# Optimization experiments

Hardware: AMD Instinct MI355X
Metric: run time of the kernel (lower is better)

## Reference

```python
import jax, jax.numpy as jnp
import numpy as np

K = 3       # attractive nearest neighbors
J = 3       # repulsive offset (uses dist[:, :, J:])
ALPHA = 0.1
NU = 1e-3


def setup_inputs() -> dict:
    key = jax.random.key(0)
    k1, k2 = jax.random.split(key, 2)
    phi_p = jax.random.normal(k1, (4, 512, 64, 64), dtype=jnp.float32)
    memory_bank = jax.random.normal(k2, (16384, 512), dtype=jnp.float32)
    r = jnp.ones((1,), dtype=jnp.float32)
    return {"phi_p": phi_p, "memory_bank": memory_bank, "r": r}


def reference(phi_p, memory_bank, r):
    B, C, H, W = phi_p.shape
    # b c h w -> b (h w) c
    x = phi_p.reshape(B, C, H * W).transpose(0, 2, 1)
    x2 = jnp.sum(x * x, axis=-1, keepdims=True)            # [B, HW, 1]
    m2 = jnp.sum(memory_bank * memory_bank, axis=-1)       # [N]
    d2 = x2 + m2[None, None, :] - 2.0 * jnp.einsum('bnc,mc->bnm', x, memory_bank)
    d2 = jnp.maximum(d2, 0.0)                              # [B, HW, N]
    # smallest K+J squared distances, ascending (topk(largest=False))
    neg_top, _ = jax.lax.top_k(-d2, K + J)
    dist = -neg_top                                        # [B, HW, K+J]
    r2 = r ** 2
    scores_att = dist[:, :, :K] - r2
    loss_att = jnp.mean(jnp.maximum(scores_att, 0.0)) / NU
    scores_rep = r2 - dist[:, :, J:] - ALPHA
    loss_rep = jnp.mean(jnp.maximum(scores_rep, 0.0)) / NU
    return loss_att + loss_rep
```

## Files before the change

### kernel.cpp

```cpp
#include <hip/hip_runtime.h>
#include <cfloat>

#define B_   4
#define C_   512
#define HW_  4096
#define R_   16384
#define N_   16384
#define ALPHA_ 0.1f
#define SCALE_ ((float)(1000.0/49152.0))

#define NCHUNK 4

typedef unsigned int u32;
typedef unsigned short u16;
typedef unsigned char u8;
typedef __attribute__((ext_vector_type(2))) unsigned long long u64x2;
typedef __attribute__((ext_vector_type(4))) float f32x4;

typedef const __attribute__((address_space(1))) u32* gas_u32;
typedef __attribute__((address_space(3))) u32* las_u32;

__device__ __forceinline__ void async16(const void* g, void* l) {
    __builtin_amdgcn_global_load_lds((gas_u32)g, (las_u32)l, 16, 0, 0);
}

__device__ __forceinline__ u32 pk_fp8x4(float a, float b, float c, float d) {
    u32 v = __builtin_amdgcn_cvt_pk_fp8_f32(a, b, 0, false);
    v = __builtin_amdgcn_cvt_pk_fp8_f32(c, d, v, true);
    return v;
}

__device__ __forceinline__ void ins6(float (&t)[6], float v) {
    if (v < t[5]) {
        t[5] = v;
        #pragma unroll
        for (int q = 5; q >= 1; --q) {
            float lo = fminf(t[q-1], t[q]);
            float hi = fmaxf(t[q-1], t[q]);
            t[q-1] = lo; t[q] = hi;
        }
    }
}

__global__ void conv_mem_kernel(const float* __restrict__ mem,
                                u8* __restrict__ Mb, float* __restrict__ m2) {
    int w = threadIdx.x >> 6, l = threadIdx.x & 63;
    int row = blockIdx.x * 4 + w;
    const float4* p = (const float4*)(mem + (size_t)row * C_);
    float4 a = p[l], b = p[l + 64];
    float s = a.x*a.x + a.y*a.y + a.z*a.z + a.w*a.w
            + b.x*b.x + b.y*b.y + b.z*b.z + b.w*b.w;
    *(u32*)(Mb + (size_t)row * C_ + l*4)       = pk_fp8x4(a.x, a.y, a.z, a.w);
    *(u32*)(Mb + (size_t)row * C_ + 256 + l*4) = pk_fp8x4(b.x, b.y, b.z, b.w);
    #pragma unroll
    for (int off = 32; off > 0; off >>= 1) s += __shfl_down(s, off);
    if (l == 0) m2[row] = s;
}

__global__ void conv_phi_kernel(const float* __restrict__ phi, u8* __restrict__ Xb,
                                float* __restrict__ x2) {
    __shared__ float T[64][65];
    int t = threadIdx.x;
    int n0 = blockIdx.x * 64, c0 = blockIdx.y * 64, b = blockIdx.z;
    const float* src = phi + ((size_t)b * C_ + c0) * HW_ + n0;
    int l = t & 63, cg = t >> 6;
    float sq = 0.f;
    #pragma unroll
    for (int p = 0; p < 16; ++p) {
        int c = cg + p * 4;
        float v = src[(size_t)c * HW_ + l];
        T[c][l] = v;
        sq = fmaf(v, v, sq);
    }
    atomicAdd(&x2[(size_t)b * HW_ + n0 + l], sq);
    __syncthreads();
    int cq = t & 15, gl0 = t >> 4;
    #pragma unroll
    for (int p = 0; p < 4; ++p) {
        int gl = gl0 + p * 16;
        u32 v = pk_fp8x4(T[cq*4+0][gl], T[cq*4+1][gl],
                         T[cq*4+2][gl], T[cq*4+3][gl]);
        size_t g = (size_t)b * HW_ + n0 + gl;
        *(u32*)(Xb + g * C_ + c0 + cq*4) = v;
    }
}

__global__ __launch_bounds__(256, 2) void gemm_topk_kernel(
    const u8* __restrict__ Xb, const u8* __restrict__ Mb,
    const float* __restrict__ m2, float* __restrict__ P ) {
    __shared__ __align__(16) u8 smem[24832];
    u8* Xs = smem;
    u8* Ms = smem + 8192;

    const int t = threadIdx.x;
    const int w = t >> 6, l = t & 63;
    const int g0  = blockIdx.x * 128;
    const int n0c = blockIdx.y * (N_ / NCHUNK);
    const int rh  = w * 32;
    const int fm  = l & 15;
    const int rq  = l >> 4;
    const int pc  = (rq ^ ((fm >> 1) & 3)) * 16;
    const int srow4 = l >> 2;
    const int soff  = (((l & 3) ^ ((l >> 3) & 3)) * 16);

    float top[8][6];
    #pragma unroll
    for (int s8 = 0; s8 < 8; ++s8)
        #pragma unroll
        for (int q = 0; q < 6; ++q) top[s8][q] = FLT_MAX;

    const u8* Xsrc = Xb + (size_t)(g0 + rh) * C_;
    u8* XsW = Xs + rh * 64;
    u8* MsW = Ms + rh * 64;

    for (int nt = 0; nt < N_ / NCHUNK / 128; ++nt) {
        const int n0 = n0c + nt * 128;
        const u8* Msrc = Mb + (size_t)(n0 + rh) * C_;

        float m2w[8];
        #pragma unroll
        for (int n = 0; n < 8; ++n) m2w[n] = m2[n0 + n * 16 + fm];

        f32x4 acc[2][8];
        #pragma unroll
        for (int m = 0; m < 2; ++m)
            #pragma unroll
            for (int n = 0; n < 8; ++n) acc[m][n] = (f32x4)0.f;

        for (int s = 0; s < 8; ++s) {
            const int k0 = s * 64;
            #pragma unroll
            for (int i = 0; i < 2; ++i) {
                async16(Xsrc + (size_t)(i*16 + srow4) * C_ + k0 + soff, XsW + i*1024);
                async16(Msrc + (size_t)(i*16 + srow4) * C_ + k0 + soff, MsW + i*1024);
            }
            __syncthreads();
            u64x2 av[2], bv[8];
            #pragma unroll
            for (int m = 0; m < 2; ++m)
                av[m] = *(const u64x2*)(Xs + (rh + m*16 + fm) * 64 + pc);
            #pragma unroll
            for (int n = 0; n < 8; ++n)
                bv[n] = *(const u64x2*)(Ms + (n*16 + fm) * 64 + pc);
            #pragma unroll
            for (int m = 0; m < 2; ++m)
                #pragma unroll
                for (int n = 0; n < 8; ++n)
                    acc[m][n] = __builtin_amdgcn_mfma_f32_16x16x32_fp8_fp8(
                        (long)av[m].x, (long)bv[n].x, acc[m][n], 0, 0, 0);
            #pragma unroll
            for (int m = 0; m < 2; ++m)
                #pragma unroll
                for (int n = 0; n < 8; ++n)
                    acc[m][n] = __builtin_amdgcn_mfma_f32_16x16x32_fp8_fp8(
                        (long)av[m].y, (long)bv[n].y, acc[m][n], 0, 0, 0);
            __syncthreads();
        }

        #pragma unroll
        for (int m = 0; m < 2; ++m)
            #pragma unroll
            for (int j = 0; j < 4; ++j) {
                float d0 = m2w[0] - 2.f * acc[m][0][j];
                float d1 = m2w[1] - 2.f * acc[m][1][j];
                float d2 = m2w[2] - 2.f * acc[m][2][j];
                float d3 = m2w[3] - 2.f * acc[m][3][j];
                float d4 = m2w[4] - 2.f * acc[m][4][j];
                float d5 = m2w[5] - 2.f * acc[m][5][j];
                float d6 = m2w[6] - 2.f * acc[m][6][j];
                float d7 = m2w[7] - 2.f * acc[m][7][j];
                float vmin = fminf(fminf(fminf(d0, d1), fminf(d2, d3)),
                                   fminf(fminf(d4, d5), fminf(d6, d7)));
                float (&tt)[6] = top[m * 4 + j];
                if (vmin < tt[5]) {
                    ins6(tt, d0); ins6(tt, d1); ins6(tt, d2); ins6(tt, d3);
                    ins6(tt, d4); ins6(tt, d5); ins6(tt, d6); ins6(tt, d7);
                }
            }
    }

    float* Mg = (float*)smem;
    #pragma unroll 1
    for (int p = 0; p < 2; ++p) {
        __syncthreads();
        if ((w >> 1) == p) {
            #pragma unroll
            for (int m = 0; m < 2; ++m)
                #pragma unroll
                for (int j = 0; j < 4; ++j) {
                    int lrow = (w & 1) * 32 + m * 16 + rq * 4 + j;
                    #pragma unroll
                    for (int q = 0; q < 6; ++q)
                        Mg[lrow * 97 + fm * 6 + q] = top[m * 4 + j][q];
                }
        }
        __syncthreads();
        if (t < 64) {
            float t6[6];
            #pragma unroll
            for (int q = 0; q < 6; ++q) t6[q] = FLT_MAX;
            const float* row = Mg + t * 97;
            for (int v = 0; v < 96; ++v) ins6(t6, row[v]);
            float* dst = P + ((size_t)(g0 + p * 64 + t) * NCHUNK + blockIdx.y) * 6;
            #pragma unroll
            for (int q = 0; q < 6; ++q) dst[q] = t6[q];
        }
    }
}

__global__ void finalize_kernel(const float* __restrict__ P, const float* __restrict__ x2,
                                const float* __restrict__ rp, float* __restrict__ out) {
    int g = blockIdx.x * 256 + threadIdx.x;
    float t6[6];
    #pragma unroll
    for (int q = 0; q < 6; ++q) t6[q] = FLT_MAX;
    const f32x4* pp = (const f32x4*)(P + (size_t)g * (NCHUNK * 6));
    #pragma unroll
    for (int q = 0; q < NCHUNK * 6 / 4; ++q) {
        f32x4 v = pp[q];
        ins6(t6, v.x); ins6(t6, v.y); ins6(t6, v.z); ins6(t6, v.w);
    }
    float x2g = x2[g];
    float rv = rp[0], r2 = rv * rv;
    float s = 0.f;
    #pragma unroll
    for (int i = 0; i < 3; ++i) {
        float d = fmaxf(t6[i] + x2g, 0.f);
        s += fmaxf(d - r2, 0.f);
    }
    #pragma unroll
    for (int i = 3; i < 6; ++i) {
        float d = fmaxf(t6[i] + x2g, 0.f);
        s += fmaxf(r2 - d - ALPHA_, 0.f);
    }
    #pragma unroll
    for (int off = 32; off > 0; off >>= 1) s += __shfl_down(s, off);
    __shared__ float red[4];
    int w = threadIdx.x >> 6, l = threadIdx.x & 63;
    if (l == 0) red[w] = s;
    __syncthreads();
    if (threadIdx.x == 0)
        atomicAdd(out, (red[0] + red[1] + red[2] + red[3]) * SCALE_);
}

#define TM 64
#define TN 64
#define KC 64
#define LDP 68

__global__ void m2_kernel(const float* __restrict__ mem, float* __restrict__ m2) {
    int wave = threadIdx.x >> 6, lane = threadIdx.x & 63;
    int row = blockIdx.x * 4 + wave;
    const float4* p = reinterpret_cast<const float4*>(mem + (size_t)row * C_);
    float4 a = p[lane], b = p[lane + 64];
    float s = a.x*a.x + a.y*a.y + a.z*a.z + a.w*a.w
            + b.x*b.x + b.y*b.y + b.z*b.z + b.w*b.w;
    #pragma unroll
    for (int off = 32; off > 0; off >>= 1) s += __shfl_down(s, off);
    if (lane == 0) m2[row] = s;
}

__global__ void x2f_kernel(const float* __restrict__ phi, float* __restrict__ x2) {
    int g = blockIdx.x * blockDim.x + threadIdx.x;
    int b = g >> 12;
    int n = g & 4095;
    const float* p = phi + (size_t)b * C_ * HW_ + n;
    float s = 0.f;
    #pragma unroll 8
    for (int c = 0; c < C_; ++c) {
        float v = p[(size_t)c * HW_];
        s = fmaf(v, v, s);
    }
    x2[g] = s;
}

__global__ __launch_bounds__(256) void dist_loss_kernel(
    const float* __restrict__ phi, const float* __restrict__ mem,
    const float* __restrict__ rp,  const float* __restrict__ m2,
    const float* __restrict__ x2,  float* __restrict__ out) {
    __shared__ float smem[2 * TM * LDP];
    float* xs = smem;
    float* ms = smem + TM * LDP;
    const int tid = threadIdx.x;
    const int tx = tid & 15, ty = tid >> 4;
    const int g0 = blockIdx.x * TM;
    const int b = g0 >> 12, n0img = g0 & 4095;
    const float* phiB = phi + (size_t)b * C_ * HW_ + n0img;
    float top[4][6];
    #pragma unroll
    for (int i = 0; i < 4; ++i)
        #pragma unroll
        for (int q = 0; q < 6; ++q) top[i][q] = FLT_MAX;
    float x2v[4];
    #pragma unroll
    for (int i = 0; i < 4; ++i) x2v[i] = x2[g0 + ty * 4 + i];
    for (int nt = 0; nt < N_ / TN; ++nt) {
        const int n0 = nt * TN;
        float acc[4][4];
        #pragma unroll
        for (int i = 0; i < 4; ++i)
            #pragma unroll
            for (int j = 0; j < 4; ++j) acc[i][j] = 0.f;
        for (int s = 0; s < C_ / KC; ++s) {
            const int k0 = s * KC;
            {
                int rr = tid & 63, cb = tid >> 6;
                #pragma unroll
                for (int p = 0; p < 16; ++p) {
                    int cc = p * 4 + cb;
                    xs[rr * LDP + cc] = phiB[(size_t)(k0 + cc) * HW_ + rr];
                }
            }
            {
                int kq = tid & 15, cb = tid >> 4;
                #pragma unroll
                for (int p = 0; p < 4; ++p) {
                    int c = p * 16 + cb;
                    float4 v = *reinterpret_cast<const float4*>(
                        mem + (size_t)(n0 + c) * C_ + k0 + kq * 4);
                    ms[(kq*4+0)*LDP + c] = v.x; ms[(kq*4+1)*LDP + c] = v.y;
                    ms[(kq*4+2)*LDP + c] = v.z; ms[(kq*4+3)*LDP + c] = v.w;
                }
            }
            __syncthreads();
            #pragma unroll
            for (int kq = 0; kq < KC / 4; ++kq) {
                float4 xa[4], mb[4];
                #pragma unroll
                for (int i = 0; i < 4; ++i)
                    xa[i] = *reinterpret_cast<const float4*>(&xs[(ty*4+i)*LDP + kq*4]);
                #pragma unroll
                for (int kk = 0; kk < 4; ++kk)
                    mb[kk] = *reinterpret_cast<const float4*>(&ms[(kq*4+kk)*LDP + tx*4]);
                #pragma unroll
                for (int i = 0; i < 4; ++i) {
                    const float xk[4] = {xa[i].x, xa[i].y, xa[i].z, xa[i].w};
                    #pragma unroll
                    for (int kk = 0; kk < 4; ++kk) {
                        const float mc[4] = {mb[kk].x, mb[kk].y, mb[kk].z, mb[kk].w};
                        #pragma unroll
                        for (int j = 0; j < 4; ++j)
                            acc[i][j] = fmaf(xk[kk], mc[j], acc[i][j]);
                    }
                }
            }
            __syncthreads();
        }
        #pragma unroll
        for (int j = 0; j < 4; ++j) {
            float m2v = m2[n0 + tx * 4 + j];
            #pragma unroll
            for (int i = 0; i < 4; ++i) {
                float d = fmaxf(x2v[i] + m2v - 2.f * acc[i][j], 0.f);
                ins6(top[i], d);
            }
        }
    }
    __syncthreads();
    float* mg = smem;
    #pragma unroll
    for (int i = 0; i < 4; ++i)
        #pragma unroll
        for (int q = 0; q < 6; ++q)
            mg[(ty*4+i)*97 + tx*6 + q] = top[i][q];
    __syncthreads();
    if (tid < 64) {
        float t6[6];
        #pragma unroll
        for (int q = 0; q < 6; ++q) t6[q] = FLT_MAX;
        const float* row = mg + tid * 97;
        for (int v = 0; v < 96; ++v) ins6(t6, row[v]);
        float rv = rp[0], r2 = rv * rv;
        float s = fmaxf(t6[0]-r2,0.f) + fmaxf(t6[1]-r2,0.f) + fmaxf(t6[2]-r2,0.f)
                + fmaxf(r2-t6[3]-ALPHA_,0.f) + fmaxf(r2-t6[4]-ALPHA_,0.f)
                + fmaxf(r2-t6[5]-ALPHA_,0.f);
        #pragma unroll
        for (int off = 32; off > 0; off >>= 1) s += __shfl_down(s, off);
        if (tid == 0) atomicAdd(out, s * SCALE_);
    }
}

extern "C" void kernel_launch(void* const* d_in, const int* in_sizes, int n_in,
                              void* d_out, int out_size, void* d_ws, size_t ws_size,
                              hipStream_t stream) {
    const float* phi = (const float*)d_in[0];
    const float* mem = (const float*)d_in[1];
    const float* rp  = (const float*)d_in[2];
    float* out = (float*)d_out;

    const size_t offX  = 0;
    const size_t offM  = (size_t)R_ * C_;
    const size_t offx2 = offM + (size_t)N_ * C_;
    const size_t offm2 = offx2 + (size_t)R_ * 4;
    const size_t offP  = offm2 + (size_t)N_ * 4;
    const size_t need  = offP + (size_t)R_ * NCHUNK * 6 * 4;

    hipMemsetAsync(out, 0, sizeof(float), stream);

    if (ws_size >= need) {
        u8*    Xb = (u8*)((char*)d_ws + offX);
        u8*    Mb = (u8*)((char*)d_ws + offM);
        float* x2 = (float*)((char*)d_ws + offx2);
        float* m2 = (float*)((char*)d_ws + offm2);
        float* P  = (float*)((char*)d_ws + offP);

        hipMemsetAsync(x2, 0, (size_t)R_ * 4, stream);
        conv_mem_kernel<<<N_ / 4, 256, 0, stream>>>(mem, Mb, m2);
        conv_phi_kernel<<<dim3(HW_ / 64, C_ / 64, B_), 256, 0, stream>>>(phi, Xb, x2);
        gemm_topk_kernel<<<dim3(128, NCHUNK), 256, 0, stream>>>(Xb, Mb, m2, P);
        finalize_kernel<<<R_ / 256, 256, 0, stream>>>(P, x2, rp, out);
    } else {
        float* m2 = (float*)d_ws;
        float* x2 = m2 + N_;
        m2_kernel<<<N_ / 4, 256, 0, stream>>>(mem, m2);
        x2f_kernel<<<R_ / 256, 256, 0, stream>>>(phi, x2);
        dist_loss_kernel<<<R_ / TM, 256, 0, stream>>>(phi, mem, rp, m2, x2, out);
    }
}
```

Before: 405.3 us.

## Swap MFMA operands so each lane owns a query row, shrink top-k state

Swaps the A/B operands of the fp8 MFMA so the accumulator layout gives each lane 4 consecutive memory-bank columns for a single query row. Each lane then keeps two top-6 lists instead of eight, which cuts register pressure. This allows launch bounds of 4 blocks per CU and a smaller shared buffer. NCHUNK doubles to 8 to expose more blocks, at the cost of a larger partial buffer and more work in the finalize pass. The m2 values are now read from global memory inside the epilogue rather than preloaded into registers.

New measurement: 451.7 us. 11.4% more time.

```diff
diff --git a/kernel.cpp b/kernel.cpp
--- a/kernel.cpp
+++ b/kernel.cpp
@@ -9,7 +9,7 @@
 #define ALPHA_ 0.1f
 #define SCALE_ ((float)(1000.0/49152.0))
 
-#define NCHUNK 4
+#define NCHUNK 8
 
 typedef unsigned int u32;
 typedef unsigned short u16;
@@ -85,10 +85,10 @@
     }
 }
 
-__global__ __launch_bounds__(256, 2) void gemm_topk_kernel(
+__global__ __launch_bounds__(256, 4) void gemm_topk_kernel(
     const u8* __restrict__ Xb, const u8* __restrict__ Mb,
     const float* __restrict__ m2, float* __restrict__ P ) {
-    __shared__ __align__(16) u8 smem[24832];
+    __shared__ __align__(16) u8 smem[16384];
     u8* Xs = smem;
     u8* Ms = smem + 8192;
 
@@ -103,11 +103,11 @@
     const int srow4 = l >> 2;
     const int soff  = (((l & 3) ^ ((l >> 3) & 3)) * 16);
 
-    float top[8][6];
-    #pragma unroll
-    for (int s8 = 0; s8 < 8; ++s8)
-        #pragma unroll
-        for (int q = 0; q < 6; ++q) top[s8][q] = FLT_MAX;
+    float top[2][6];
+    #pragma unroll
+    for (int m = 0; m < 2; ++m)
+        #pragma unroll
+        for (int q = 0; q < 6; ++q) top[m][q] = FLT_MAX;
 
     const u8* Xsrc = Xb + (size_t)(g0 + rh) * C_;
     u8* XsW = Xs + rh * 64;
@@ -117,15 +117,11 @@
         const int n0 = n0c + nt * 128;
         const u8* Msrc = Mb + (size_t)(n0 + rh) * C_;
 
-        float m2w[8];
-        #pragma unroll
-        for (int n = 0; n < 8; ++n) m2w[n] = m2[n0 + n * 16 + fm];
-
         f32x4 acc[2][8];
         #pragma unroll
         for (int m = 0; m < 2; ++m)
             #pragma unroll
-            for (int n = 0; n < 8; ++n) acc[m][n] = (f32x4)0.f;
+            for (int a = 0; a < 8; ++a) acc[m][a] = (f32x4)0.f;
 
         for (int s = 0; s < 8; ++s) {
             const int k0 = s * 64;
@@ -135,48 +131,52 @@
                 async16(Msrc + (size_t)(i*16 + srow4) * C_ + k0 + soff, MsW + i*1024);
             }
             __syncthreads();
-            u64x2 av[2], bv[8];
+            u64x2 xv[2];
             #pragma unroll
             for (int m = 0; m < 2; ++m)
-                av[m] = *(const u64x2*)(Xs + (rh + m*16 + fm) * 64 + pc);
-            #pragma unroll
-            for (int n = 0; n < 8; ++n)
-                bv[n] = *(const u64x2*)(Ms + (n*16 + fm) * 64 + pc);
-            #pragma unroll
-            for (int m = 0; m < 2; ++m)
-                #pragma unroll
-                for (int n = 0; n < 8; ++n)
-                    acc[m][n] = __builtin_amdgcn_mfma_f32_16x16x32_fp8_fp8(
-                        (long)av[m].x, (long)bv[n].x, acc[m][n], 0, 0, 0);
-            #pragma unroll
-            for (int m = 0; m < 2; ++m)
-                #pragma unroll
-                for (int n = 0; n < 8; ++n)
-                    acc[m][n] = __builtin_amdgcn_mfma_f32_16x16x32_fp8_fp8(
-                        (long)av[m].y, (long)bv[n].y, acc[m][n], 0, 0, 0);
+                xv[m] = *(const u64x2*)(Xs + (rh + m*16 + fm) * 64 + pc);
+            #pragma unroll
+            for (int a = 0; a < 8; ++a) {
+                u64x2 av = *(const u64x2*)(Ms + (a*16 + fm) * 64 + pc);
+                #pragma unroll
+                for (int m = 0; m < 2; ++m) {
+                    acc[m][a] = __builtin_amdgcn_mfma_f32_16x16x32_fp8_fp8(
+                        (long)av.x, (long)xv[m].x, acc[m][a], 0, 0, 0);
+                    acc[m][a] = __builtin_amdgcn_mfma_f32_16x16x32_fp8_fp8(
+                        (long)av.y, (long)xv[m].y, acc[m][a], 0, 0, 0);
+                }
+            }
             __syncthreads();
         }
 
-        #pragma unroll
-        for (int m = 0; m < 2; ++m)
-            #pragma unroll
-            for (int j = 0; j < 4; ++j) {
-                float d0 = m2w[0] - 2.f * acc[m][0][j];
-                float d1 = m2w[1] - 2.f * acc[m][1][j];
-                float d2 = m2w[2] - 2.f * acc[m][2][j];
-                float d3 = m2w[3] - 2.f * acc[m][3][j];
-                float d4 = m2w[4] - 2.f * acc[m][4][j];
-                float d5 = m2w[5] - 2.f * acc[m][5][j];
-                float d6 = m2w[6] - 2.f * acc[m][6][j];
-                float d7 = m2w[7] - 2.f * acc[m][7][j];
-                float vmin = fminf(fminf(fminf(d0, d1), fminf(d2, d3)),
-                                   fminf(fminf(d4, d5), fminf(d6, d7)));
-                float (&tt)[6] = top[m * 4 + j];
-                if (vmin < tt[5]) {
-                    ins6(tt, d0); ins6(tt, d1); ins6(tt, d2); ins6(tt, d3);
-                    ins6(tt, d4); ins6(tt, d5); ins6(tt, d6); ins6(tt, d7);
-                }
-            }
+        float vm0 = FLT_MAX, vm1 = FLT_MAX;
+        #pragma unroll
+        for (int a = 0; a < 8; ++a) {
+            float4 q = *(const float4*)(m2 + n0 + a * 16 + rq * 4);
+            f32x4 a0 = acc[0][a], a1 = acc[1][a];
+            vm0 = fminf(vm0, fminf(fminf(q.x - 2.f*a0.x, q.y - 2.f*a0.y),
+                                   fminf(q.z - 2.f*a0.z, q.w - 2.f*a0.w)));
+            vm1 = fminf(vm1, fminf(fminf(q.x - 2.f*a1.x, q.y - 2.f*a1.y),
+                                   fminf(q.z - 2.f*a1.z, q.w - 2.f*a1.w)));
+        }
+        if (vm0 < top[0][5]) {
+            #pragma unroll
+            for (int a = 0; a < 8; ++a) {
+                float4 q = *(const float4*)(m2 + n0 + a * 16 + rq * 4);
+                f32x4 a0 = acc[0][a];
+                ins6(top[0], q.x - 2.f*a0.x); ins6(top[0], q.y - 2.f*a0.y);
+                ins6(top[0], q.z - 2.f*a0.z); ins6(top[0], q.w - 2.f*a0.w);
+            }
+        }
+        if (vm1 < top[1][5]) {
+            #pragma unroll
+            for (int a = 0; a < 8; ++a) {
+                float4 q = *(const float4*)(m2 + n0 + a * 16 + rq * 4);
+                f32x4 a1 = acc[1][a];
+                ins6(top[1], q.x - 2.f*a1.x); ins6(top[1], q.y - 2.f*a1.y);
+                ins6(top[1], q.z - 2.f*a1.z); ins6(top[1], q.w - 2.f*a1.w);
+            }
+        }
     }
 
     float* Mg = (float*)smem;
@@ -185,22 +185,21 @@
         __syncthreads();
         if ((w >> 1) == p) {
             #pragma unroll
-            for (int m = 0; m < 2; ++m)
-                #pragma unroll
-                for (int j = 0; j < 4; ++j) {
-                    int lrow = (w & 1) * 32 + m * 16 + rq * 4 + j;
-                    #pragma unroll
-                    for (int q = 0; q < 6; ++q)
-                        Mg[lrow * 97 + fm * 6 + q] = top[m * 4 + j][q];
-                }
+            for (int m = 0; m < 2; ++m) {
+                int lrow = (w & 1) * 32 + m * 16 + fm;
+                #pragma unroll
+                for (int q = 0; q < 6; ++q)
+                    Mg[lrow * 25 + rq * 6 + q] = top[m][q];
+            }
         }
         __syncthreads();
         if (t < 64) {
             float t6[6];
             #pragma unroll
             for (int q = 0; q < 6; ++q) t6[q] = FLT_MAX;
-            const float* row = Mg + t * 97;
-            for (int v = 0; v < 96; ++v) ins6(t6, row[v]);
+            const float* row = Mg + t * 25;
+            #pragma unroll
+            for (int v = 0; v < 24; ++v) ins6(t6, row[v]);
             float* dst = P + ((size_t)(g0 + p * 64 + t) * NCHUNK + blockIdx.y) * 6;
             #pragma unroll
             for (int q = 0; q < 6; ++q) dst[q] = t6[q];
```
